# Performance work log

Measured on AMD Instinct MI355X. Metric: run time of the kernel, lower is better.

Reference implementation:

```python
import jax, jax.numpy as jnp
import numpy as np

HIDDEN = 2048
N_HEADS = 32
N_KV_HEADS = 8
HEAD_DIM = HIDDEN // N_HEADS  # 64
ROPE_BASE = 10000.0
B, S = 2, 2048
NEG_INF = -1e9


def rotate_half(x):
    x1, x2 = jnp.split(x, 2, axis=-1)
    return jnp.concatenate((-x2, x1), axis=-1)


def rope_cos_sin(seq_len, head_dim, base, dtype):
    inv_freq = 1.0 / (base ** (jnp.arange(0, head_dim, 2, dtype=jnp.float32) / head_dim))
    pos = jnp.arange(seq_len, dtype=jnp.float32)
    freqs = jnp.outer(pos, inv_freq)              # [S, D/2]
    emb = jnp.concatenate((freqs, freqs), axis=-1)  # [S, D]
    return jnp.cos(emb).astype(dtype)[None, None], jnp.sin(emb).astype(dtype)[None, None]


def setup_inputs() -> dict:
    key = jax.random.key(0)
    ks = jax.random.split(key, 5)
    hidden_states = jax.random.normal(ks[0], (B, S, HIDDEN), dtype=jnp.float32)
    # causal additive mask, Llama-style
    causal = jnp.tril(jnp.ones((S, S), dtype=bool))
    attention_mask = jnp.where(causal, 0.0, NEG_INF).astype(jnp.float32)
    attention_mask = jnp.broadcast_to(attention_mask[None, None], (B, 1, S, S))
    sc = 1.0 / np.sqrt(HIDDEN)
    Wq = jax.random.normal(ks[1], (HIDDEN, HIDDEN), dtype=jnp.float32) * sc
    Wk = jax.random.normal(ks[2], (N_KV_HEADS * HEAD_DIM, HIDDEN), dtype=jnp.float32) * sc
    Wv = jax.random.normal(ks[3], (N_KV_HEADS * HEAD_DIM, HIDDEN), dtype=jnp.float32) * sc
    Wo = jax.random.normal(ks[4], (HIDDEN, HIDDEN), dtype=jnp.float32) * sc
    return {"hidden_states": hidden_states, "attention_mask": attention_mask,
            "Wq": Wq, "Wk": Wk, "Wv": Wv, "Wo": Wo}


def reference(hidden_states, attention_mask, Wq, Wk, Wv, Wo):
    b, s, _ = hidden_states.shape
    groups = N_HEADS // N_KV_HEADS
    # projections (torch Linear: x @ W.T)
    q = (hidden_states @ Wq.T).reshape(b, s, N_HEADS, HEAD_DIM).transpose(0, 2, 1, 3)      # [b,H,s,d]
    k = (hidden_states @ Wk.T).reshape(b, s, N_KV_HEADS, HEAD_DIM).transpose(0, 2, 1, 3)   # [b,Hk,s,d]
    v = (hidden_states @ Wv.T).reshape(b, s, N_KV_HEADS, HEAD_DIM).transpose(0, 2, 1, 3)
    cos, sin = rope_cos_sin(s, HEAD_DIM, ROPE_BASE, hidden_states.dtype)
    q = q * cos + rotate_half(q) * sin
    k = k * cos + rotate_half(k) * sin
    # GQA without materializing repeated K/V: view q as [b, Hk, g, s, d]
    qg = q.reshape(b, N_KV_HEADS, groups, s, HEAD_DIM)
    scores = jnp.einsum('bhgqd,bhkd->bhgqk', qg, k) / np.sqrt(HEAD_DIM)  # [b,Hk,g,s,s]
    scores = scores + attention_mask[:, :, None]                          # mask [b,1,1,s,s]
    probs = jax.nn.softmax(scores.astype(jnp.float32), axis=-1).astype(q.dtype)
    attn = jnp.einsum('bhgqk,bhkd->bhgqd', probs, v)                      # [b,Hk,g,s,d]
    attn = attn.reshape(b, N_HEADS, s, HEAD_DIM).transpose(0, 2, 1, 3).reshape(b, s, HIDDEN)
    return attn @ Wo.T
```

## Files before the change

### kernel.cpp

```cpp
#include <hip/hip_runtime.h>
#include <math.h>

#define HID 2048
#define NH 32
#define NKV 8
#define HD 64
#define BB 2
#define SS 2048
#define MTOT (BB * SS)

typedef __bf16 bf16;
typedef __bf16 bf16x8 __attribute__((ext_vector_type(8)));
typedef __bf16 bf16x4 __attribute__((ext_vector_type(4)));
typedef float f32x4 __attribute__((ext_vector_type(4)));

#define MFMA16(a, b, c) __builtin_amdgcn_mfma_f32_16x16x32_bf16((a), (b), (c), 0, 0, 0)

__device__ __forceinline__ void load_lds16(const void* g, void* l) {
  __builtin_amdgcn_global_load_lds((const __attribute__((address_space(1))) void*)g,
                                   (__attribute__((address_space(3))) void*)l, 16, 0, 0);
}

__global__ void cvt_kernel(const float* __restrict__ src, bf16* __restrict__ dst, int n) {
  int i = (blockIdx.x * 256 + threadIdx.x) * 4;
  if (i >= n) return;
  float4 v = *(const float4*)(src + i);
  bf16x4 o;
  o[0] = (bf16)v.x; o[1] = (bf16)v.y; o[2] = (bf16)v.z; o[3] = (bf16)v.w;
  *(bf16x4*)(dst + i) = o;
}

__device__ __forceinline__ void gemm128_core(const bf16* __restrict__ Ap,
                                             const bf16* __restrict__ Wp,
                                             bf16* As, bf16* Bs, f32x4 acc[4][4]) {
  const int tid = threadIdx.x;
  const int w = tid >> 6, lane = tid & 63;
  const int sr = lane >> 2;
  const int scc = (lane & 3) * 8;
  const int l16 = lane & 15, quad = lane >> 4;
  const int mw = (w >> 1) * 64, nw = (w & 1) * 64;

  const bf16* gA = Ap + (size_t)(w * 32 + sr) * HID + scc;
  const bf16* gB = Wp + (size_t)(w * 32 + sr) * HID + scc;
  bf16* lA = As + (w * 32) * 32;
  bf16* lB = Bs + (w * 32) * 32;

  for (int k0 = 0; k0 < HID; k0 += 32) {
    load_lds16(gA + k0, lA);
    load_lds16(gA + k0 + (size_t)16 * HID, lA + 16 * 32);
    load_lds16(gB + k0, lB);
    load_lds16(gB + k0 + (size_t)16 * HID, lB + 16 * 32);
    __syncthreads();
    bf16x8 af[4], bfr[4];
#pragma unroll
    for (int mi = 0; mi < 4; ++mi)
      af[mi] = *(const bf16x8*)&As[(mw + mi * 16 + l16) * 32 + quad * 8];
#pragma unroll
    for (int ni = 0; ni < 4; ++ni)
      bfr[ni] = *(const bf16x8*)&Bs[(nw + ni * 16 + l16) * 32 + quad * 8];
#pragma unroll
    for (int mi = 0; mi < 4; ++mi)
#pragma unroll
      for (int ni = 0; ni < 4; ++ni)
        acc[mi][ni] = MFMA16(af[mi], bfr[ni], acc[mi][ni]);
    __syncthreads();
  }
}

#define QSCALE 0.1803368801f
__global__ __launch_bounds__(256) void gemm_qkv(const bf16* __restrict__ A,
                                                const bf16* __restrict__ Wq,
                                                const bf16* __restrict__ Wk,
                                                const bf16* __restrict__ Wv,
                                                bf16* __restrict__ Qb,
                                                bf16* __restrict__ Kb,
                                                bf16* __restrict__ Vt) {
  __shared__ bf16 As[128 * 32];
  __shared__ bf16 Bs[128 * 32];
  const int tileM = blockIdx.x * 128;
  const int n0 = blockIdx.y * 128;
  const bf16* Wp;
  int mode;
  if (n0 < HID) { Wp = Wq + (size_t)n0 * HID; mode = 0; }
  else if (n0 < HID + 512) { Wp = Wk + (size_t)(n0 - HID) * HID; mode = 1; }
  else { Wp = Wv + (size_t)(n0 - HID - 512) * HID; mode = 2; }

  f32x4 acc[4][4];
#pragma unroll
  for (int i = 0; i < 4; ++i)
#pragma unroll
    for (int j = 0; j < 4; ++j) acc[i][j] = (f32x4){0.f, 0.f, 0.f, 0.f};

  gemm128_core(A + (size_t)tileM * HID, Wp, As, Bs, acc);

  const int tid = threadIdx.x;
  const int w = tid >> 6, lane = tid & 63;
  const int l16 = lane & 15, quad = lane >> 4;
  const int mw = (w >> 1) * 64, nw = (w & 1) * 64;
#pragma unroll
  for (int mi = 0; mi < 4; ++mi) {
#pragma unroll
    for (int ni = 0; ni < 4; ++ni) {
#pragma unroll
      for (int r = 0; r < 4; ++r) {
        int grow = tileM + mw + mi * 16 + quad * 4 + r;
        int gcol = n0 + nw + ni * 16 + l16;
        float v = acc[mi][ni][r];
        int b = grow >> 11, spos = grow & (SS - 1);
        if (mode == 0) {
          Qb[(size_t)grow * HID + gcol] = (bf16)(v * QSCALE);
        } else if (mode == 1) {
          int nk = gcol - HID;
          Kb[(((size_t)(b * NKV + (nk >> 6))) * SS + spos) * HD + (nk & 63)] = (bf16)v;
        } else {
          int nv = gcol - HID - 512;
          Vt[(((size_t)(b * NKV + (nv >> 6))) * HD + (nv & 63)) * SS + spos] = (bf16)v;
        }
      }
    }
  }
}

__global__ __launch_bounds__(256) void gemm_out(const bf16* __restrict__ A,
                                                const bf16* __restrict__ Wo,
                                                float* __restrict__ out) {
  __shared__ bf16 As[128 * 32];
  __shared__ bf16 Bs[128 * 32];
  const int tileM = blockIdx.x * 128;
  const int n0 = blockIdx.y * 128;
  f32x4 acc[4][4];
#pragma unroll
  for (int i = 0; i < 4; ++i)
#pragma unroll
    for (int j = 0; j < 4; ++j) acc[i][j] = (f32x4){0.f, 0.f, 0.f, 0.f};

  gemm128_core(A + (size_t)tileM * HID, Wo + (size_t)n0 * HID, As, Bs, acc);

  const int tid = threadIdx.x;
  const int w = tid >> 6, lane = tid & 63;
  const int l16 = lane & 15, quad = lane >> 4;
  const int mw = (w >> 1) * 64, nw = (w & 1) * 64;
#pragma unroll
  for (int mi = 0; mi < 4; ++mi)
#pragma unroll
    for (int ni = 0; ni < 4; ++ni)
#pragma unroll
      for (int r = 0; r < 4; ++r) {
        int grow = tileM + mw + mi * 16 + quad * 4 + r;
        int gcol = n0 + nw + ni * 16 + l16;
        out[(size_t)grow * HID + gcol] = acc[mi][ni][r];
      }
}

__global__ void rope_q(bf16* __restrict__ Qb) {
  int idx = blockIdx.x * 256 + threadIdx.x;
  int i = idx & 31;
  int h = (idx >> 5) & 31;
  int spos = (idx >> 10) & (SS - 1);
  int b = idx >> 21;
  bf16* p = Qb + ((size_t)(b * SS + spos)) * HID + h * HD;
  float x1 = (float)p[i], x2 = (float)p[i + 32];
  float ex = (float)i * (1.0f / 32.0f);
  float inv = 1.0f / powf(10000.0f, ex);
  float fr = (float)spos * inv;
  float sn, cs;
  sincosf(fr, &sn, &cs);
  p[i] = (bf16)(x1 * cs - x2 * sn);
  p[i + 32] = (bf16)(x2 * cs + x1 * sn);
}

__global__ void rope_k(bf16* __restrict__ Kb) {
  int idx = blockIdx.x * 256 + threadIdx.x;
  int i = idx & 31;
  int spos = (idx >> 5) & (SS - 1);
  int kvh = (idx >> 16) & 7;
  int b = idx >> 19;
  bf16* p = Kb + (((size_t)(b * NKV + kvh)) * SS + spos) * HD;
  float x1 = (float)p[i], x2 = (float)p[i + 32];
  float ex = (float)i * (1.0f / 32.0f);
  float inv = 1.0f / powf(10000.0f, ex);
  float fr = (float)spos * inv;
  float sn, cs;
  sincosf(fr, &sn, &cs);
  p[i] = (bf16)(x1 * cs - x2 * sn);
  p[i + 32] = (bf16)(x2 * cs + x1 * sn);
}

#define PSTR 72
__global__ __launch_bounds__(256, 3) void attn(const bf16* __restrict__ Qb,
                                               const bf16* __restrict__ Kb,
                                               const bf16* __restrict__ Vt,
                                               bf16* __restrict__ Ctx) {
  __shared__ bf16 Ktile[2][64 * 64];
  __shared__ bf16 Vtile[2][64 * 64];
  __shared__ bf16 Pbuf[4][16 * PSTR];
  const int tid = threadIdx.x;
  const int w = tid >> 6, lane = tid & 63;
  const int l16 = lane & 15, quad = lane >> 4;
  const int bh = blockIdx.y, b = bh >> 5, h = bh & 31, kvh = h >> 2;
  bf16* Pw = &Pbuf[w][0];
  const char* Kslice = (const char*)(Kb + ((size_t)(b * NKV + kvh)) * SS * HD);
  const char* Vslice = (const char*)(Vt + ((size_t)(b * NKV + kvh)) * HD * SS);
  const int qrel = w * 16 + l16;

  const int srow = (lane >> 3) & 7;
  const int pchunk = ((lane & 7) ^ srow) << 4;
  const int so = ((quad ^ (l16 & 7)) << 4);
  const int so2 = so ^ 64;

  const int qtA = (int)blockIdx.x;

  int cur = 0;
  {
#pragma unroll
    for (int i = 0; i < 2; ++i) {
      const int r = w * 16 + i * 8 + srow;
      load_lds16(Kslice + (size_t)r * 128 + pchunk,
                 (char*)Ktile[0] + (w * 16 + i * 8) * 128);
      load_lds16(Vslice + (size_t)r * 4096 + pchunk,
                 (char*)Vtile[0] + (w * 16 + i * 8) * 128);
    }
  }

  for (int t = 0; t < 2; ++t) {
    const int qt = t ? (31 - qtA) : qtA;
    const int q = qt * 64 + qrel;

    const bf16* Qp = Qb + ((size_t)(b * SS + q)) * HID + h * HD + quad * 8;
    bf16x8 qb0 = *(const bf16x8*)Qp;
    bf16x8 qb1 = *(const bf16x8*)(Qp + 32);

    float l = 0.f;
    f32x4 oacc[4];
#pragma unroll
    for (int d = 0; d < 4; ++d) oacc[d] = (f32x4){0.f, 0.f, 0.f, 0.f};

    for (int kt = 0; kt <= qt; ++kt) {
      __syncthreads();

      const bool have_next = (kt < qt) || (t == 0);
      if (have_next) {
        const int nkb = (kt < qt) ? (kt + 1) * 64 : 0;
        const int nb = cur ^ 1;
#pragma unroll
        for (int i = 0; i < 2; ++i) {
          const int r = w * 16 + i * 8 + srow;
          load_lds16(Kslice + (size_t)(nkb + r) * 128 + pchunk,
                     (char*)Ktile[nb] + (w * 16 + i * 8) * 128);
          load_lds16(Vslice + (size_t)r * 4096 + (size_t)nkb * 2 + pchunk,
                     (char*)Vtile[nb] + (w * 16 + i * 8) * 128);
        }
      }

      const char* Kc = (const char*)Ktile[cur] + l16 * 128;
      const char* Vc = (const char*)Vtile[cur] + l16 * 128;
      const bool diag = (kt == qt);

#pragma unroll
      for (int nt = 0; nt < 4; ++nt) {
        bf16x8 kf0 = *(const bf16x8*)(Kc + nt * 2048 + so);
        bf16x8 kf1 = *(const bf16x8*)(Kc + nt * 2048 + so2);
        f32x4 s = {0.f, 0.f, 0.f, 0.f};
        s = MFMA16(kf0, qb0, s);
        s = MFMA16(kf1, qb1, s);
        bf16x4 pk;
        if (diag) {
          const int krel = nt * 16 + quad * 4;
#pragma unroll
          for (int r = 0; r < 4; ++r) {
            float p = (krel + r > qrel) ? 0.f : __builtin_amdgcn_exp2f(s[r]);
            l += p;
            pk[r] = (bf16)p;
          }
        } else {
#pragma unroll
          for (int r = 0; r < 4; ++r) {
            float p = __builtin_amdgcn_exp2f(s[r]);
            l += p;
            pk[r] = (bf16)p;
          }
        }
        *(bf16x4*)&Pw[l16 * PSTR + nt * 16 + quad * 4] = pk;
      }

      bf16x8 p0 = *(const bf16x8*)&Pw[l16 * PSTR + quad * 8];
      bf16x8 p1 = *(const bf16x8*)&Pw[l16 * PSTR + 32 + quad * 8];
#pragma unroll
      for (int dn = 0; dn < 4; ++dn) {
        bf16x8 v0 = *(const bf16x8*)(Vc + dn * 2048 + so);
        bf16x8 v1 = *(const bf16x8*)(Vc + dn * 2048 + so2);
        oacc[dn] = MFMA16(v0, p0, oacc[dn]);
        oacc[dn] = MFMA16(v1, p1, oacc[dn]);
      }
      cur ^= 1;
    }

    l += __shfl_xor(l, 16);
    l += __shfl_xor(l, 32);
    const float inv = 1.0f / l;
    bf16* Cp = Ctx + ((size_t)(b * SS + q)) * HID + h * HD + quad * 4;
#pragma unroll
    for (int dn = 0; dn < 4; ++dn) {
      bf16x4 ov;
#pragma unroll
      for (int r = 0; r < 4; ++r) ov[r] = (bf16)(oacc[dn][r] * inv);
      *(bf16x4*)(Cp + dn * 16) = ov;
    }
  }
}

extern "C" void kernel_launch(void* const* d_in, const int* in_sizes, int n_in,
                              void* d_out, int out_size, void* d_ws, size_t ws_size,
                              hipStream_t stream) {
  const float* hs = (const float*)d_in[0];
  const float* Wq = (const float*)d_in[2];
  const float* Wk = (const float*)d_in[3];
  const float* Wv = (const float*)d_in[4];
  const float* Wo = (const float*)d_in[5];

  char* ws = (char*)d_ws;
  bf16* A_b  = (bf16*)(ws);
  bf16* Wq_b = (bf16*)(ws + 16777216);
  bf16* Wk_b = (bf16*)(ws + 25165824);
  bf16* Wv_b = (bf16*)(ws + 27262976);
  bf16* Wo_b = (bf16*)(ws + 29360128);
  bf16* Qb   = (bf16*)(ws + 37748736);
  bf16* Kb   = (bf16*)(ws + 54525952);
  bf16* Vt   = (bf16*)(ws + 58720256);
  bf16* Ctx  = A_b;

  cvt_kernel<<<8192, 256, 0, stream>>>(hs, A_b, MTOT * HID);
  cvt_kernel<<<4096, 256, 0, stream>>>(Wq, Wq_b, HID * HID);
  cvt_kernel<<<1024, 256, 0, stream>>>(Wk, Wk_b, 512 * HID);
  cvt_kernel<<<1024, 256, 0, stream>>>(Wv, Wv_b, 512 * HID);
  cvt_kernel<<<4096, 256, 0, stream>>>(Wo, Wo_b, HID * HID);

  gemm_qkv<<<dim3(MTOT / 128, 24), 256, 0, stream>>>(A_b, Wq_b, Wk_b, Wv_b, Qb, Kb, Vt);
  rope_q<<<16384, 256, 0, stream>>>(Qb);
  rope_k<<<4096, 256, 0, stream>>>(Kb);
  attn<<<dim3(16, BB * NH), 256, 0, stream>>>(Qb, Kb, Vt, Ctx);
  gemm_out<<<dim3(MTOT / 128, HID / 128), 256, 0, stream>>>(Ctx, Wo_b, (float*)d_out);
}
```

Measured before the change: 346.9 us.

## Fuse RoPE into QKV GEMM epilogue and merge conversion kernels

Applies rotary embedding to Q and K directly on the fp32 accumulators in the QKV GEMM epilogue, pairing column fragments 0/2 and 1/3 of each 64-wide head. This removes the separate rope_q and rope_k kernels and their extra read and write passes over Q and K. The five fp32-to-bf16 conversion launches are also merged into one kernel. In exchange, the epilogue now does sincos work, and RoPE is applied before the bf16 rounding, which changes numerics slightly.

```diff
diff --git a/kernel.cpp b/kernel.cpp
--- a/kernel.cpp
+++ b/kernel.cpp
@@ -21,9 +21,21 @@
                                    (__attribute__((address_space(3))) void*)l, 16, 0, 0);
 }
 
-__global__ void cvt_kernel(const float* __restrict__ src, bf16* __restrict__ dst, int n) {
-  int i = (blockIdx.x * 256 + threadIdx.x) * 4;
-  if (i >= n) return;
+__global__ void cvt_all(const float* __restrict__ hs, const float* __restrict__ Wq,
+                        const float* __restrict__ Wk, const float* __restrict__ Wv,
+                        const float* __restrict__ Wo,
+                        bf16* __restrict__ A_b, bf16* __restrict__ Wq_b,
+                        bf16* __restrict__ Wk_b, bf16* __restrict__ Wv_b,
+                        bf16* __restrict__ Wo_b) {
+  int bid = blockIdx.x;
+  const float* src;
+  bf16* dst;
+  if (bid < 8192)       { src = hs; dst = A_b; }
+  else if (bid < 12288) { src = Wq; dst = Wq_b; bid -= 8192; }
+  else if (bid < 13312) { src = Wk; dst = Wk_b; bid -= 12288; }
+  else if (bid < 14336) { src = Wv; dst = Wv_b; bid -= 13312; }
+  else                  { src = Wo; dst = Wo_b; bid -= 14336; }
+  int i = (bid * 256 + threadIdx.x) * 4;
   float4 v = *(const float4*)(src + i);
   bf16x4 o;
   o[0] = (bf16)v.x; o[1] = (bf16)v.y; o[2] = (bf16)v.z; o[3] = (bf16)v.w;
@@ -68,6 +80,7 @@
 }
 
 #define QSCALE 0.1803368801f
+#define L2B 0.4152410118f
 __global__ __launch_bounds__(256) void gemm_qkv(const bf16* __restrict__ A,
                                                 const bf16* __restrict__ Wq,
                                                 const bf16* __restrict__ Wk,
@@ -97,24 +110,52 @@
   const int w = tid >> 6, lane = tid & 63;
   const int l16 = lane & 15, quad = lane >> 4;
   const int mw = (w >> 1) * 64, nw = (w & 1) * 64;
-#pragma unroll
-  for (int mi = 0; mi < 4; ++mi) {
-#pragma unroll
-    for (int ni = 0; ni < 4; ++ni) {
+
+  if (mode == 2) {
+#pragma unroll
+    for (int mi = 0; mi < 4; ++mi)
+#pragma unroll
+      for (int ni = 0; ni < 4; ++ni)
+#pragma unroll
+        for (int r = 0; r < 4; ++r) {
+          int grow = tileM + mw + mi * 16 + quad * 4 + r;
+          int gcol = n0 + nw + ni * 16 + l16;
+          int b = grow >> 11, spos = grow & (SS - 1);
+          int nv = gcol - HID - 512;
+          Vt[(((size_t)(b * NKV + (nv >> 6))) * HD + (nv & 63)) * SS + spos] =
+              (bf16)acc[mi][ni][r];
+        }
+  } else {
+    const float inv0 = __builtin_amdgcn_exp2f(-(float)l16 * L2B);
+    const float inv1 = __builtin_amdgcn_exp2f(-(float)(l16 + 16) * L2B);
+#pragma unroll
+    for (int mi = 0; mi < 4; ++mi) {
 #pragma unroll
       for (int r = 0; r < 4; ++r) {
         int grow = tileM + mw + mi * 16 + quad * 4 + r;
-        int gcol = n0 + nw + ni * 16 + l16;
-        float v = acc[mi][ni][r];
         int b = grow >> 11, spos = grow & (SS - 1);
+        float sn0, cs0, sn1, cs1;
+        sincosf((float)spos * inv0, &sn0, &cs0);
+        sincosf((float)spos * inv1, &sn1, &cs1);
+        float a0 = acc[mi][0][r], a1 = acc[mi][1][r];
+        float a2 = acc[mi][2][r], a3 = acc[mi][3][r];
+        float o0 = a0 * cs0 - a2 * sn0;
+        float o2 = a2 * cs0 + a0 * sn0;
+        float o1 = a1 * cs1 - a3 * sn1;
+        float o3 = a3 * cs1 + a1 * sn1;
         if (mode == 0) {
-          Qb[(size_t)grow * HID + gcol] = (bf16)(v * QSCALE);
-        } else if (mode == 1) {
-          int nk = gcol - HID;
-          Kb[(((size_t)(b * NKV + (nk >> 6))) * SS + spos) * HD + (nk & 63)] = (bf16)v;
+          bf16* qp = Qb + (size_t)grow * HID + n0 + nw + l16;
+          qp[0]  = (bf16)(o0 * QSCALE);
+          qp[16] = (bf16)(o1 * QSCALE);
+          qp[32] = (bf16)(o2 * QSCALE);
+          qp[48] = (bf16)(o3 * QSCALE);
         } else {
-          int nv = gcol - HID - 512;
-          Vt[(((size_t)(b * NKV + (nv >> 6))) * HD + (nv & 63)) * SS + spos] = (bf16)v;
+          int kvh = (n0 - HID + nw) >> 6;
+          bf16* kp = Kb + ((size_t)(b * NKV + kvh) * SS + spos) * HD + l16;
+          kp[0]  = (bf16)o0;
+          kp[16] = (bf16)o1;
+          kp[32] = (bf16)o2;
+          kp[48] = (bf16)o3;
         }
       }
     }
@@ -150,40 +191,6 @@
         int gcol = n0 + nw + ni * 16 + l16;
         out[(size_t)grow * HID + gcol] = acc[mi][ni][r];
       }
-}
-
-__global__ void rope_q(bf16* __restrict__ Qb) {
-  int idx = blockIdx.x * 256 + threadIdx.x;
-  int i = idx & 31;
-  int h = (idx >> 5) & 31;
-  int spos = (idx >> 10) & (SS - 1);
-  int b = idx >> 21;
-  bf16* p = Qb + ((size_t)(b * SS + spos)) * HID + h * HD;
-  float x1 = (float)p[i], x2 = (float)p[i + 32];
-  float ex = (float)i * (1.0f / 32.0f);
-  float inv = 1.0f / powf(10000.0f, ex);
-  float fr = (float)spos * inv;
-  float sn, cs;
-  sincosf(fr, &sn, &cs);
-  p[i] = (bf16)(x1 * cs - x2 * sn);
-  p[i + 32] = (bf16)(x2 * cs + x1 * sn);
-}
-
-__global__ void rope_k(bf16* __restrict__ Kb) {
-  int idx = blockIdx.x * 256 + threadIdx.x;
-  int i = idx & 31;
-  int spos = (idx >> 5) & (SS - 1);
-  int kvh = (idx >> 16) & 7;
-  int b = idx >> 19;
-  bf16* p = Kb + (((size_t)(b * NKV + kvh)) * SS + spos) * HD;
-  float x1 = (float)p[i], x2 = (float)p[i + 32];
-  float ex = (float)i * (1.0f / 32.0f);
-  float inv = 1.0f / powf(10000.0f, ex);
-  float fr = (float)spos * inv;
-  float sn, cs;
-  sincosf(fr, &sn, &cs);
-  p[i] = (bf16)(x1 * cs - x2 * sn);
-  p[i + 32] = (bf16)(x2 * cs + x1 * sn);
 }
 
 #define PSTR 72
@@ -329,15 +336,8 @@
   bf16* Vt   = (bf16*)(ws + 58720256);
   bf16* Ctx  = A_b;
 
-  cvt_kernel<<<8192, 256, 0, stream>>>(hs, A_b, MTOT * HID);
-  cvt_kernel<<<4096, 256, 0, stream>>>(Wq, Wq_b, HID * HID);
-  cvt_kernel<<<1024, 256, 0, stream>>>(Wk, Wk_b, 512 * HID);
-  cvt_kernel<<<1024, 256, 0, stream>>>(Wv, Wv_b, 512 * HID);
-  cvt_kernel<<<4096, 256, 0, stream>>>(Wo, Wo_b, HID * HID);
-
+  cvt_all<<<18432, 256, 0, stream>>>(hs, Wq, Wk, Wv, Wo, A_b, Wq_b, Wk_b, Wv_b, Wo_b);
   gemm_qkv<<<dim3(MTOT / 128, 24), 256, 0, stream>>>(A_b, Wq_b, Wk_b, Wv_b, Qb, Kb, Vt);
-  rope_q<<<16384, 256, 0, stream>>>(Qb);
-  rope_k<<<4096, 256, 0, stream>>>(Kb);
   attn<<<dim3(16, BB * NH), 256, 0, stream>>>(Qb, Kb, Vt, Ctx);
   gemm_out<<<dim3(MTOT / 128, HID / 128), 256, 0, stream>>>(Ctx, Wo_b, (float*)d_out);
 }
```

Result: faster. 338.6 us (-2.4%).
